# Performance work log

Hardware: AMD Instinct MI355X
Metric: run time of the kernel (lower is better)

## Reference

```python
import jax, jax.numpy as jnp
import numpy as np

TEMP = 0.07
MAX_SAMPLES = 2048
RADIUS = 10
HARD_FRAC = 0.75
FG_LABEL = 1
B, C, H, W = 8, 64, 256, 256
BLOCK = 32

MAX_FG = MAX_SAMPLES // 2                      # 1024
NEG_BUDGET = MAX_SAMPLES - MAX_FG              # 1024
HARD_BUDGET = int(round(HARD_FRAC * NEG_BUDGET))  # 768
RAND_BUDGET = NEG_BUDGET - HARD_BUDGET         # 256


def setup_inputs() -> dict:
    key = jax.random.key(0)
    feats = jax.random.normal(key, (B, C, H, W), dtype=jnp.float32)
    # 32x32-block checkerboard labels: guarantees abundant fg / ring / interior-bg pools
    ii, jj = jnp.meshgrid(jnp.arange(H), jnp.arange(W), indexing='ij')
    lbl = (((ii // BLOCK) + (jj // BLOCK)) % 2).astype(jnp.int32)
    labels = jnp.broadcast_to(lbl, (B, H, W))
    return {"feats": feats, "labels": labels}


def _forward(feats, labels):
    Bn, Cn, Hn, Wn = feats.shape
    n_pix = Hn * Wn
    f_flat = feats.reshape(Bn, Cn, n_pix).transpose(0, 2, 1)  # [B, P, C]
    l_flat = labels.reshape(Bn, n_pix)

    fg = labels == FG_LABEL                                   # [B, H, W]
    k = 2 * RADIUS + 1
    # max-pool dilation of fg mask (kernel k, stride 1, pad RADIUS == SAME)
    dil = jax.lax.reduce_window(fg.astype(jnp.float32), -jnp.inf, jax.lax.max,
                                (1, k, k), (1, 1, 1), 'SAME') > 0.0
    fg_flat = fg.reshape(Bn, n_pix)
    bg_flat = ~fg_flat                                        # all pixels valid (no ignore)
    ring_flat = dil.reshape(Bn, n_pix) & ~fg_flat & bg_flat
    bgonly_flat = bg_flat & ~ring_flat

    def per_image(f, y, fgm, ringm, bgm, key):
        k1, k2, k3 = jax.random.split(key, 3)
        def pick(mask, kk, n):
            # random subset of n true positions (== randperm[:n] in distribution)
            s = jnp.where(mask, jax.random.uniform(kk, mask.shape), -1.0)
            return jax.lax.top_k(s, n)[1]
        idx = jnp.concatenate([pick(fgm, k1, MAX_FG),
                               pick(ringm, k2, HARD_BUDGET),
                               pick(bgm, k3, RAND_BUDGET)])    # [K]
        fs = f[idx]                                            # [K, C]
        ys = y[idx]
        fs = fs / jnp.maximum(jnp.linalg.norm(fs, axis=1, keepdims=True), 1e-12)
        logits = fs @ fs.T / TEMP                              # [K, K]
        logits = logits - jax.lax.stop_gradient(logits.max(axis=1, keepdims=True))
        eye = jnp.eye(MAX_SAMPLES, dtype=bool)
        pos = (ys[:, None] == ys[None, :]) & ~eye
        exp_l = jnp.exp(logits) * (~eye)
        denom = jnp.maximum(exp_l.sum(axis=1), 1e-8)
        pos_sum = jnp.maximum(jnp.where(pos, exp_l, 0.0).sum(axis=1), 1e-8)
        valid = pos.any(axis=1) & (ys == FG_LABEL)
        loss_terms = -jnp.log(pos_sum / denom)
        n_valid = jnp.maximum(valid.sum(), 1)
        return jnp.where(valid, loss_terms, 0.0).sum() / n_valid

    keys = jax.random.split(jax.random.key(1), Bn)
    losses = jax.vmap(per_image)(f_flat, l_flat, fg_flat, ring_flat, bgonly_flat, keys)
    return losses.mean()


def reference(feats, labels):
    return _forward(feats, labels)
```

## Files before the change

### kernel.cpp

```cpp
#include <hip/hip_runtime.h>
#include <stdint.h>

#define NPIX   65536
#define NIMG   8
#define NCH    64
#define KSEL   2048
#define NFG    1024
#define NRING  768
#define NBG    256
#define INV_TEMP 14.285714285714286f

typedef __attribute__((ext_vector_type(8))) short bf16x8;
typedef __attribute__((ext_vector_type(4))) float f32x4;

__device__ __forceinline__ void tf2x32(uint32_t k0, uint32_t k1,
                                       uint32_t& x0, uint32_t& x1) {
  const uint32_t ks2 = k0 ^ k1 ^ 0x1BD11BDAu;
  x0 += k0; x1 += k1;
#define TF_RND(r) { x0 += x1; x1 = (x1 << (r)) | (x1 >> (32 - (r))); x1 ^= x0; }
  TF_RND(13) TF_RND(15) TF_RND(26) TF_RND(6)
  x0 += k1;  x1 += ks2 + 1u;
  TF_RND(17) TF_RND(29) TF_RND(16) TF_RND(24)
  x0 += ks2; x1 += k0 + 2u;
  TF_RND(13) TF_RND(15) TF_RND(26) TF_RND(6)
  x0 += k0;  x1 += k1 + 3u;
  TF_RND(17) TF_RND(29) TF_RND(16) TF_RND(24)
  x0 += k1;  x1 += ks2 + 4u;
  TF_RND(13) TF_RND(15) TF_RND(26) TF_RND(6)
  x0 += ks2; x1 += k0 + 5u;
#undef TF_RND
}

__device__ __forceinline__ ushort f2bf(float f) {
  uint32_t u = __float_as_uint(f);
  return (ushort)((u + 0x7FFFu + ((u >> 16) & 1u)) >> 16);
}

#define ZERO_F4 1552
__global__ __launch_bounds__(1024) void dilate_pack(const int* __restrict__ labels,
                                                    uint64_t* __restrict__ fgw,
                                                    uint64_t* __restrict__ dilw,
                                                    float4* __restrict__ zregion,
                                                    uint32_t* __restrict__ keys,
                                                    float* __restrict__ out) {
  __shared__ uint64_t fgs[336], hds[336];
  const int tid = threadIdx.x;
  const int img = blockIdx.x >> 2;
  const int r0 = (blockIdx.x & 3) * 64;

  if (blockIdx.x == 0) {
    for (int t = tid; t < ZERO_F4; t += 1024)
      zregion[t] = make_float4(0.f, 0.f, 0.f, 0.f);
  } else if (blockIdx.x == 1 && tid == 0) {
    out[0] = 0.0f;
    for (int b = 0; b < NIMG; ++b) {
      uint32_t kb0 = 0u, kb1 = (uint32_t)b;
      tf2x32(0u, 1u, kb0, kb1);
      for (int g = 0; g < 3; ++g) {
        uint32_t x0 = 0u, x1 = (uint32_t)g;
        tf2x32(kb0, kb1, x0, x1);
        keys[(b * 3 + g) * 2 + 0] = x0;
        keys[(b * 3 + g) * 2 + 1] = x1;
      }
    }
  }

  #pragma unroll
  for (int it = 0; it < 21; ++it) {
    int li = it * 1024 + tid;
    int hr = r0 - 10 + (li >> 8);
    int col = li & 255;
    bool bit = false;
    if (hr >= 0 && hr < 256) bit = (labels[(img << 16) + (hr << 8) + col] == 1);
    uint64_t m = __ballot(bit);
    if ((tid & 63) == 0) fgs[li >> 6] = m;
  }
  __syncthreads();

  for (int w = tid; w < 336; w += 1024) {
    int wc = w & 3;
    uint64_t x = fgs[w];
    uint64_t L = wc > 0 ? fgs[w - 1] : 0ull;
    uint64_t R = wc < 3 ? fgs[w + 1] : 0ull;
    uint64_t acc = x;
    #pragma unroll
    for (int s = 1; s <= 10; ++s) {
      acc |= (x << s) | (L >> (64 - s));
      acc |= (x >> s) | (R << (64 - s));
    }
    hds[w] = acc;
  }
  __syncthreads();

  for (int w = tid; w < 256; w += 1024) {
    int r = w >> 2, wc = w & 3;
    int gr = r0 + r;
    uint64_t acc = 0ull;
    #pragma unroll
    for (int dr = 0; dr <= 20; ++dr) acc |= hds[(r + dr) * 4 + wc];
    fgw[img * 1024 + gr * 4 + wc]  = fgs[(r + 10) * 4 + wc];
    dilw[img * 1024 + gr * 4 + wc] = acc;
  }
}

__global__ __launch_bounds__(256) void hash_hist(const uint64_t* __restrict__ fgw,
                                                 const uint64_t* __restrict__ dilw,
                                                 const uint32_t* __restrict__ keys,
                                                 uint32_t* __restrict__ mgrp,
                                                 uint32_t* __restrict__ hist) {
  __shared__ uint32_t lh[768];
  __shared__ uint64_t fgl[32], dll[32];
  const int tid = threadIdx.x;
  for (int t = tid; t < 768; t += 256) lh[t] = 0;
  const int b = blockIdx.x >> 5;
  const int base = blockIdx.x * 2048;
  const int w0 = (blockIdx.x & 31) * 32;
  if (tid < 32) fgl[tid] = fgw[b * 1024 + w0 + tid];
  else if (tid < 64) dll[tid - 32] = dilw[b * 1024 + w0 + tid - 32];
  const uint32_t K00 = keys[b * 6 + 0], K01 = keys[b * 6 + 1];
  const uint32_t K10 = keys[b * 6 + 2], K11 = keys[b * 6 + 3];
  const uint32_t K20 = keys[b * 6 + 4], K21 = keys[b * 6 + 5];
  __syncthreads();

  #pragma unroll
  for (int k = 0; k < 8; ++k) {
    int off = k * 256 + tid;
    int pix = (base + off) & 65535;
    int lw = off >> 6, bp = off & 63;
    uint32_t fgbit = (uint32_t)((fgl[lw] >> bp) & 1ull);
    uint32_t dilbit = (uint32_t)((dll[lw] >> bp) & 1ull);
    uint32_t grp = fgbit ? 0u : (dilbit ? 1u : 2u);
    uint32_t k0 = grp == 0 ? K00 : grp == 1 ? K10 : K20;
    uint32_t k1 = grp == 0 ? K01 : grp == 1 ? K11 : K21;
    uint32_t x0 = 0u, x1 = (uint32_t)pix;
    tf2x32(k0, k1, x0, x1);
    uint32_t m = (x0 ^ x1) >> 9;
    mgrp[base + off] = (m << 2) | grp;
    atomicAdd(&lh[grp * 256 + (m >> 15)], 1u);
  }
  __syncthreads();
  for (int t = tid; t < 768; t += 256)
    if (lh[t]) atomicAdd(&hist[b * 768 + t], lh[t]);
}

__global__ __launch_bounds__(256) void topk_emit(const uint32_t* __restrict__ mgrp,
                                                 const uint32_t* __restrict__ hist,
                                                 uint32_t* __restrict__ TG,
                                                 uint32_t* __restrict__ cnt,
                                                 uint32_t* __restrict__ candcnt,
                                                 unsigned long long* __restrict__ cand,
                                                 int* __restrict__ idx_out) {
  __shared__ uint32_t hh[768];
  __shared__ uint32_t sT[3], loc[3], lbd[3], basA[3], basB[3];
  const int tid = threadIdx.x;
  const int b = blockIdx.x >> 5;
  const int base = blockIdx.x * 2048;
  for (int t = tid; t < 768; t += 256) hh[t] = hist[b * 768 + t];
  if (tid < 3) { loc[tid] = 0; lbd[tid] = 0; }
  __syncthreads();

  if (tid < 3) {
    uint32_t nsel = tid == 0 ? NFG : tid == 1 ? NRING : NBG;
    const uint32_t* h = hh + tid * 256;
    uint32_t cum = 0; int T = 255;
    for (; T > 0; --T) {
      uint32_t c = h[T];
      if (cum + c >= nsel) break;
      cum += c;
    }
    sT[tid] = (uint32_t)T;
    if ((blockIdx.x & 31) == 0) {
      TG[(b * 3 + tid) * 2] = (uint32_t)T;
      TG[(b * 3 + tid) * 2 + 1] = cum;
    }
  }
  __syncthreads();
  const uint32_t T0 = sT[0], T1 = sT[1], T2 = sT[2];

  #pragma unroll
  for (int k = 0; k < 8; ++k) {
    uint32_t v = mgrp[base + k * 256 + tid];
    uint32_t g = v & 3u, bin = v >> 17;
    uint32_t T = g == 0 ? T0 : g == 1 ? T1 : T2;
    if (bin > T) atomicAdd(&loc[g], 1u);
    else if (bin == T) atomicAdd(&lbd[g], 1u);
  }
  __syncthreads();
  if (tid < 3) {
    basA[tid] = atomicAdd(&cnt[b * 3 + tid], loc[tid]);
    basB[tid] = atomicAdd(&candcnt[b * 3 + tid], lbd[tid]);
    loc[tid] = 0; lbd[tid] = 0;
  }
  __syncthreads();

  #pragma unroll
  for (int k = 0; k < 8; ++k) {
    int p = base + k * 256 + tid;
    uint32_t v = mgrp[p];
    uint32_t g = v & 3u, bin = v >> 17;
    uint32_t T = g == 0 ? T0 : g == 1 ? T1 : T2;
    int pix = p & 65535;
    if (bin > T) {
      uint32_t o = atomicAdd(&loc[g], 1u);
      int seg = g == 0 ? 0 : g == 1 ? NFG : (NFG + NRING);
      idx_out[b * KSEL + seg + (int)(basA[g] + o)] = pix;
    } else if (bin == T) {
      uint32_t o = atomicAdd(&lbd[g], 1u);
      uint32_t c = basB[g] + o;
      uint32_t m = v >> 2;
      if (c < 1024u)
        cand[(b * 3 + g) * 1024 + c] = ((unsigned long long)m << 16) | (uint32_t)pix;
    }
  }
}

#define GA 16
__global__ __launch_bounds__(256) void gather_rank_t(
    const float* __restrict__ feats, const int* __restrict__ idx,
    const uint32_t* __restrict__ TG, const uint32_t* __restrict__ candcnt,
    const unsigned long long* __restrict__ cand, ushort* __restrict__ fs) {
  __shared__ float tile[GA * 65];
  __shared__ float ssb[16 * GA];
  __shared__ float sscale[GA];
  __shared__ int lidx[GA];
  __shared__ unsigned long long cb[1024];
  const int tid = threadIdx.x;
  const int img = blockIdx.x >> 7;
  const int win = (blockIdx.x & 127) * GA;
  int seg, segoff, nsel;
  if (win < NFG)               { seg = 0; segoff = 0;            nsel = NFG; }
  else if (win < NFG + NRING)  { seg = 1; segoff = NFG;          nsel = NRING; }
  else                         { seg = 2; segoff = NFG + NRING;  nsel = NBG; }
  const int task = img * 3 + seg;
  const uint32_t G = TG[task * 2 + 1];
  const int poslo = win - segoff;

  if (tid < GA) {
    if ((uint32_t)(poslo + tid) < G)
      lidx[tid] = idx[img * KSEL + win + tid];
  }
  const bool needRank = (uint32_t)(poslo + GA) > G;
  if (needRank) {
    const int c = (int)(candcnt[task] < 1024u ? candcnt[task] : 1024u);
    const int r = nsel - (int)G;
    for (int i = tid; i < c; i += 256) cb[i] = cand[task * 1024 + i];
    __syncthreads();
    for (int i = tid; i < c; i += 256) {
      unsigned long long me = cb[i];
      uint32_t mm = (uint32_t)(me >> 16), pi = (uint32_t)(me & 0xFFFFu);
      int rank = 0;
      for (int j = 0; j < c; ++j) {
        unsigned long long o = cb[j];
        uint32_t om = (uint32_t)(o >> 16), op = (uint32_t)(o & 0xFFFFu);
        if (om > mm || (om == mm && op < pi)) ++rank;
      }
      if (rank < r) {
        int slot = (int)G + rank - poslo;
        if (slot >= 0 && slot < GA) lidx[slot] = (int)pi;
      }
    }
  }
  __syncthreads();

  const int a = tid & 15, q = tid >> 4;
  const int pix = lidx[a];
  const float* fb = feats + ((size_t)img * NCH + q * 4) * NPIX + pix;
  float ss = 0.f;
  #pragma unroll
  for (int k = 0; k < 4; ++k) {
    float v = fb[(size_t)k * NPIX];
    tile[a * 65 + q * 4 + k] = v;
    ss += v * v;
  }
  ssb[q * GA + a] = ss;
  __syncthreads();
  if (q == 0) {
    float tot = 0.f;
    #pragma unroll
    for (int q2 = 0; q2 < 16; ++q2) tot += ssb[q2 * GA + a];
    sscale[a] = 1.0f / fmaxf(sqrtf(tot), 1e-12f);
  }
  __syncthreads();

  const int row = tid >> 4, c4 = tid & 15;
  const float sc = sscale[row];
  ushort4 v4;
  v4.x = f2bf(tile[row * 65 + c4 * 4 + 0] * sc);
  v4.y = f2bf(tile[row * 65 + c4 * 4 + 1] * sc);
  v4.z = f2bf(tile[row * 65 + c4 * 4 + 2] * sc);
  v4.w = f2bf(tile[row * 65 + c4 * 4 + 3] * sc);
  ((ushort4*)(fs + ((size_t)img * KSEL + win + row) * NCH))[c4] = v4;
}

__global__ __launch_bounds__(256) void loss_mfma(const ushort* __restrict__ fs,
                                                 float* __restrict__ out) {
  const int img = blockIdx.x & 7;
  const int a0 = (blockIdx.x >> 3) * 32;
  const ushort* X = fs + (size_t)img * KSEL * NCH;
  const int tid = threadIdx.x;
  const int lane = tid & 63, wave = tid >> 6;
  const int quad = lane >> 4, col = lane & 15;
  const int rt = wave >> 1, colh = wave & 1;

  __shared__ float redD[2][2][16];
  __shared__ float redP[2][16];

  const int arow = a0 + rt * 16 + col;
  const bf16x8* Ap = (const bf16x8*)(X + (size_t)arow * NCH + quad * 8);
  const bf16x8 a_lo = Ap[0];
  const bf16x8 a_hi = Ap[4];

  float pD[4] = {0.f, 0.f, 0.f, 0.f};
  float pP[4] = {0.f, 0.f, 0.f, 0.f};
  const int ct0 = colh * 64;
  const int mbase = a0 + rt * 16 + quad * 4;

  for (int ct = ct0; ct < ct0 + 64; ++ct) {
    const int j = ct * 16 + col;
    const bf16x8* Bp = (const bf16x8*)(X + (size_t)j * NCH + quad * 8);
    bf16x8 b_lo = Bp[0];
    bf16x8 b_hi = Bp[4];
    f32x4 d = {0.f, 0.f, 0.f, 0.f};
    d = __builtin_amdgcn_mfma_f32_16x16x32_bf16(a_lo, b_lo, d, 0, 0, 0);
    d = __builtin_amdgcn_mfma_f32_16x16x32_bf16(a_hi, b_hi, d, 0, 0, 0);
    #pragma unroll
    for (int r = 0; r < 4; ++r) {
      float e = __expf(d[r] * INV_TEMP);
      if (j == mbase + r) e = 0.f;
      pD[r] += e;
      if (colh == 0) pP[r] += e;
    }
  }

  #pragma unroll
  for (int o = 1; o < 16; o <<= 1) {
    #pragma unroll
    for (int r = 0; r < 4; ++r) {
      pD[r] += __shfl_xor(pD[r], o);
      pP[r] += __shfl_xor(pP[r], o);
    }
  }
  if (col == 0) {
    #pragma unroll
    for (int r = 0; r < 4; ++r) {
      redD[rt][colh][quad * 4 + r] = pD[r];
      if (colh == 0) redP[rt][quad * 4 + r] = pP[r];
    }
  }
  __syncthreads();

  float term = 0.f;
  if (tid < 32) {
    int lrt = tid >> 4, lr = tid & 15;
    float dsum = fmaxf(redD[lrt][0][lr] + redD[lrt][1][lr], 1e-8f);
    float psum = fmaxf(redP[lrt][lr], 1e-8f);
    term = __logf(dsum) - __logf(psum);
  }
  if (tid < 64) {
    #pragma unroll
    for (int o = 32; o > 0; o >>= 1) term += __shfl_xor(term, o);
    if (tid == 0) atomicAdd(out, term * (1.0f / (NFG * NIMG)));
  }
}

extern "C" void kernel_launch(void* const* d_in, const int* in_sizes, int n_in,
                              void* d_out, int out_size, void* d_ws, size_t ws_size,
                              hipStream_t stream) {
  const float* feats = (const float*)d_in[0];
  const int* labels  = (const int*)d_in[1];
  float* out = (float*)d_out;

  char* ws = (char*)d_ws;
  uint64_t* fgw     = (uint64_t*)(ws);
  uint64_t* dilw    = (uint64_t*)(ws + 65536);
  uint32_t* keys    = (uint32_t*)(ws + 131072);
  uint32_t* TG      = (uint32_t*)(ws + 131328);
  uint32_t* hist    = (uint32_t*)(ws + 131584);
  uint32_t* cnt     = (uint32_t*)(ws + 156160);
  uint32_t* candcnt = (uint32_t*)(ws + 156288);
  unsigned long long* cand = (unsigned long long*)(ws + 156416);
  int*      idx     = (int*)(ws + 353024);
  uint32_t* mgrp    = (uint32_t*)(ws + 524288);
  ushort*   fs      = (ushort*)(ws + 2621440);

  hipLaunchKernelGGL(dilate_pack, dim3(32), dim3(1024), 0, stream,
                     labels, fgw, dilw, (float4*)hist, keys, out);
  hipLaunchKernelGGL(hash_hist, dim3(NIMG * 32), dim3(256), 0, stream,
                     fgw, dilw, keys, mgrp, hist);
  hipLaunchKernelGGL(topk_emit, dim3(NIMG * 32), dim3(256), 0, stream,
                     mgrp, hist, TG, cnt, candcnt, cand, idx);
  hipLaunchKernelGGL(gather_rank_t, dim3((NIMG * KSEL) / GA), dim3(256), 0, stream,
                     feats, idx, TG, candcnt, cand, fs);
  hipLaunchKernelGGL(loss_mfma, dim3(NIMG * (NFG / 32)), dim3(256), 0, stream,
                     fs, out);
}
```

Baseline: 243.9 us.

## Fuse dilation with hash histogram and recompute hashes in top-k emit

Merges the dilation and hash-histogram kernels into one launch that writes per-block partial histograms, and drops the global atomics on the histogram. The per-pixel mgrp buffer is removed: topk_emit recomputes the Threefry hash from the fg/dilation bitmasks instead of reading stored values. This cuts one kernel launch and the 2 MB mgrp write/read, at the cost of doing the hash twice. The fused kernel runs only 32 blocks of 1024 threads, so the hash histogram now runs on far fewer CUs than the 256 blocks used before.

```diff
diff --git a/kernel.cpp b/kernel.cpp
--- a/kernel.cpp
+++ b/kernel.cpp
@@ -31,39 +31,39 @@
 #undef TF_RND
 }
 
+__device__ __forceinline__ void img_keys(int img, uint32_t* k6) {
+  uint32_t kb0 = 0u, kb1 = (uint32_t)img;
+  tf2x32(0u, 1u, kb0, kb1);
+  #pragma unroll
+  for (int g = 0; g < 3; ++g) {
+    uint32_t x0 = 0u, x1 = (uint32_t)g;
+    tf2x32(kb0, kb1, x0, x1);
+    k6[g * 2] = x0; k6[g * 2 + 1] = x1;
+  }
+}
+
 __device__ __forceinline__ ushort f2bf(float f) {
   uint32_t u = __float_as_uint(f);
   return (ushort)((u + 0x7FFFu + ((u >> 16) & 1u)) >> 16);
 }
 
-#define ZERO_F4 1552
-__global__ __launch_bounds__(1024) void dilate_pack(const int* __restrict__ labels,
-                                                    uint64_t* __restrict__ fgw,
-                                                    uint64_t* __restrict__ dilw,
-                                                    float4* __restrict__ zregion,
-                                                    uint32_t* __restrict__ keys,
-                                                    float* __restrict__ out) {
-  __shared__ uint64_t fgs[336], hds[336];
+__global__ __launch_bounds__(1024) void dilate_hash_hist(
+    const int* __restrict__ labels, uint64_t* __restrict__ fgw,
+    uint64_t* __restrict__ dilw, uint32_t* __restrict__ histpart,
+    uint32_t* __restrict__ zsmall, float* __restrict__ out) {
+  __shared__ uint64_t fgs[336], hds[336], dls[256];
+  __shared__ uint32_t lh[768];
+  __shared__ uint32_t sk[6];
   const int tid = threadIdx.x;
   const int img = blockIdx.x >> 2;
   const int r0 = (blockIdx.x & 3) * 64;
 
   if (blockIdx.x == 0) {
-    for (int t = tid; t < ZERO_F4; t += 1024)
-      zregion[t] = make_float4(0.f, 0.f, 0.f, 0.f);
-  } else if (blockIdx.x == 1 && tid == 0) {
-    out[0] = 0.0f;
-    for (int b = 0; b < NIMG; ++b) {
-      uint32_t kb0 = 0u, kb1 = (uint32_t)b;
-      tf2x32(0u, 1u, kb0, kb1);
-      for (int g = 0; g < 3; ++g) {
-        uint32_t x0 = 0u, x1 = (uint32_t)g;
-        tf2x32(kb0, kb1, x0, x1);
-        keys[(b * 3 + g) * 2 + 0] = x0;
-        keys[(b * 3 + g) * 2 + 1] = x1;
-      }
-    }
-  }
+    if (tid < 64) zsmall[tid] = 0u;
+    if (tid == 0) out[0] = 0.0f;
+  }
+  if (tid == 0) img_keys(img, (uint32_t*)sk);
+  for (int t = tid; t < 768; t += 1024) lh[t] = 0;
 
   #pragma unroll
   for (int it = 0; it < 21; ++it) {
@@ -92,70 +92,60 @@
   }
   __syncthreads();
 
-  for (int w = tid; w < 256; w += 1024) {
-    int r = w >> 2, wc = w & 3;
-    int gr = r0 + r;
+  if (tid < 256) {
+    int r = tid >> 2, wc = tid & 3;
     uint64_t acc = 0ull;
     #pragma unroll
     for (int dr = 0; dr <= 20; ++dr) acc |= hds[(r + dr) * 4 + wc];
-    fgw[img * 1024 + gr * 4 + wc]  = fgs[(r + 10) * 4 + wc];
-    dilw[img * 1024 + gr * 4 + wc] = acc;
-  }
-}
-
-__global__ __launch_bounds__(256) void hash_hist(const uint64_t* __restrict__ fgw,
-                                                 const uint64_t* __restrict__ dilw,
-                                                 const uint32_t* __restrict__ keys,
-                                                 uint32_t* __restrict__ mgrp,
-                                                 uint32_t* __restrict__ hist) {
-  __shared__ uint32_t lh[768];
-  __shared__ uint64_t fgl[32], dll[32];
-  const int tid = threadIdx.x;
-  for (int t = tid; t < 768; t += 256) lh[t] = 0;
-  const int b = blockIdx.x >> 5;
-  const int base = blockIdx.x * 2048;
-  const int w0 = (blockIdx.x & 31) * 32;
-  if (tid < 32) fgl[tid] = fgw[b * 1024 + w0 + tid];
-  else if (tid < 64) dll[tid - 32] = dilw[b * 1024 + w0 + tid - 32];
-  const uint32_t K00 = keys[b * 6 + 0], K01 = keys[b * 6 + 1];
-  const uint32_t K10 = keys[b * 6 + 2], K11 = keys[b * 6 + 3];
-  const uint32_t K20 = keys[b * 6 + 4], K21 = keys[b * 6 + 5];
-  __syncthreads();
-
-  #pragma unroll
-  for (int k = 0; k < 8; ++k) {
-    int off = k * 256 + tid;
-    int pix = (base + off) & 65535;
-    int lw = off >> 6, bp = off & 63;
-    uint32_t fgbit = (uint32_t)((fgl[lw] >> bp) & 1ull);
-    uint32_t dilbit = (uint32_t)((dll[lw] >> bp) & 1ull);
+    dls[tid] = acc;
+    fgw[img * 1024 + (r0 + r) * 4 + wc]  = fgs[(r + 10) * 4 + wc];
+    dilw[img * 1024 + (r0 + r) * 4 + wc] = acc;
+  }
+  __syncthreads();
+
+  const uint32_t K0a = sk[0], K0b = sk[1], K1a = sk[2], K1b = sk[3],
+                 K2a = sk[4], K2b = sk[5];
+  #pragma unroll
+  for (int it = 0; it < 16; ++it) {
+    int li = it * 1024 + tid;
+    int r = li >> 8, col = li & 255;
+    int wc = col >> 6, bp = col & 63;
+    uint32_t fgbit = (uint32_t)((fgs[(r + 10) * 4 + wc] >> bp) & 1ull);
+    uint32_t dilbit = (uint32_t)((dls[r * 4 + wc] >> bp) & 1ull);
     uint32_t grp = fgbit ? 0u : (dilbit ? 1u : 2u);
-    uint32_t k0 = grp == 0 ? K00 : grp == 1 ? K10 : K20;
-    uint32_t k1 = grp == 0 ? K01 : grp == 1 ? K11 : K21;
-    uint32_t x0 = 0u, x1 = (uint32_t)pix;
+    uint32_t k0 = grp == 0 ? K0a : grp == 1 ? K1a : K2a;
+    uint32_t k1 = grp == 0 ? K0b : grp == 1 ? K1b : K2b;
+    uint32_t x0 = 0u, x1 = (uint32_t)(((r0 + r) << 8) | col);
     tf2x32(k0, k1, x0, x1);
     uint32_t m = (x0 ^ x1) >> 9;
-    mgrp[base + off] = (m << 2) | grp;
     atomicAdd(&lh[grp * 256 + (m >> 15)], 1u);
   }
   __syncthreads();
-  for (int t = tid; t < 768; t += 256)
-    if (lh[t]) atomicAdd(&hist[b * 768 + t], lh[t]);
-}
-
-__global__ __launch_bounds__(256) void topk_emit(const uint32_t* __restrict__ mgrp,
-                                                 const uint32_t* __restrict__ hist,
-                                                 uint32_t* __restrict__ TG,
-                                                 uint32_t* __restrict__ cnt,
-                                                 uint32_t* __restrict__ candcnt,
-                                                 unsigned long long* __restrict__ cand,
-                                                 int* __restrict__ idx_out) {
+  for (int t = tid; t < 768; t += 1024)
+    histpart[blockIdx.x * 768 + t] = lh[t];
+}
+
+__global__ __launch_bounds__(256) void topk_emit(
+    const uint64_t* __restrict__ fgw, const uint64_t* __restrict__ dilw,
+    const uint32_t* __restrict__ histpart, uint32_t* __restrict__ TG,
+    uint32_t* __restrict__ cnt, uint32_t* __restrict__ candcnt,
+    unsigned long long* __restrict__ cand, int* __restrict__ idx_out) {
   __shared__ uint32_t hh[768];
+  __shared__ uint64_t fgl[32], dll[32];
+  __shared__ uint32_t sk[6];
   __shared__ uint32_t sT[3], loc[3], lbd[3], basA[3], basB[3];
   const int tid = threadIdx.x;
   const int b = blockIdx.x >> 5;
   const int base = blockIdx.x * 2048;
-  for (int t = tid; t < 768; t += 256) hh[t] = hist[b * 768 + t];
+  const int w0 = (blockIdx.x & 31) * 32;
+
+  for (int t = tid; t < 768; t += 256) {
+    const uint32_t* hp = histpart + (b * 4) * 768 + t;
+    hh[t] = hp[0] + hp[768] + hp[1536] + hp[2304];
+  }
+  if (tid == 0) img_keys(b, (uint32_t*)sk);
+  if (tid < 32) fgl[tid] = fgw[b * 1024 + w0 + tid];
+  else if (tid < 64) dll[tid - 32] = dilw[b * 1024 + w0 + tid - 32];
   if (tid < 3) { loc[tid] = 0; lbd[tid] = 0; }
   __syncthreads();
 
@@ -175,15 +165,26 @@
     }
   }
   __syncthreads();
-  const uint32_t T0 = sT[0], T1 = sT[1], T2 = sT[2];
-
+
+  uint32_t mv[8]; uint32_t gv[8];
+  const uint32_t K0a = sk[0], K0b = sk[1], K1a = sk[2], K1b = sk[3],
+                 K2a = sk[4], K2b = sk[5];
   #pragma unroll
   for (int k = 0; k < 8; ++k) {
-    uint32_t v = mgrp[base + k * 256 + tid];
-    uint32_t g = v & 3u, bin = v >> 17;
-    uint32_t T = g == 0 ? T0 : g == 1 ? T1 : T2;
-    if (bin > T) atomicAdd(&loc[g], 1u);
-    else if (bin == T) atomicAdd(&lbd[g], 1u);
+    int off = k * 256 + tid;
+    int lw = off >> 6, bp = off & 63;
+    uint32_t fgbit = (uint32_t)((fgl[lw] >> bp) & 1ull);
+    uint32_t dilbit = (uint32_t)((dll[lw] >> bp) & 1ull);
+    uint32_t grp = fgbit ? 0u : (dilbit ? 1u : 2u);
+    uint32_t k0 = grp == 0 ? K0a : grp == 1 ? K1a : K2a;
+    uint32_t k1 = grp == 0 ? K0b : grp == 1 ? K1b : K2b;
+    uint32_t x0 = 0u, x1 = (uint32_t)((base + off) & 65535);
+    tf2x32(k0, k1, x0, x1);
+    uint32_t m = (x0 ^ x1) >> 9;
+    mv[k] = m; gv[k] = grp;
+    uint32_t T = sT[grp], bin = m >> 15;
+    if (bin > T) atomicAdd(&loc[grp], 1u);
+    else if (bin == T) atomicAdd(&lbd[grp], 1u);
   }
   __syncthreads();
   if (tid < 3) {
@@ -195,11 +196,9 @@
 
   #pragma unroll
   for (int k = 0; k < 8; ++k) {
-    int p = base + k * 256 + tid;
-    uint32_t v = mgrp[p];
-    uint32_t g = v & 3u, bin = v >> 17;
-    uint32_t T = g == 0 ? T0 : g == 1 ? T1 : T2;
-    int pix = p & 65535;
+    uint32_t m = mv[k], g = gv[k];
+    uint32_t T = sT[g], bin = m >> 15;
+    int pix = (base + k * 256 + tid) & 65535;
     if (bin > T) {
       uint32_t o = atomicAdd(&loc[g], 1u);
       int seg = g == 0 ? 0 : g == 1 ? NFG : (NFG + NRING);
@@ -207,7 +206,6 @@
     } else if (bin == T) {
       uint32_t o = atomicAdd(&lbd[g], 1u);
       uint32_t c = basB[g] + o;
-      uint32_t m = v >> 2;
       if (c < 1024u)
         cand[(b * 3 + g) * 1024 + c] = ((unsigned long long)m << 16) | (uint32_t)pix;
     }
@@ -371,24 +369,20 @@
   float* out = (float*)d_out;
 
   char* ws = (char*)d_ws;
-  uint64_t* fgw     = (uint64_t*)(ws);
-  uint64_t* dilw    = (uint64_t*)(ws + 65536);
-  uint32_t* keys    = (uint32_t*)(ws + 131072);
-  uint32_t* TG      = (uint32_t*)(ws + 131328);
-  uint32_t* hist    = (uint32_t*)(ws + 131584);
-  uint32_t* cnt     = (uint32_t*)(ws + 156160);
-  uint32_t* candcnt = (uint32_t*)(ws + 156288);
-  unsigned long long* cand = (unsigned long long*)(ws + 156416);
-  int*      idx     = (int*)(ws + 353024);
-  uint32_t* mgrp    = (uint32_t*)(ws + 524288);
-  ushort*   fs      = (ushort*)(ws + 2621440);
-
-  hipLaunchKernelGGL(dilate_pack, dim3(32), dim3(1024), 0, stream,
-                     labels, fgw, dilw, (float4*)hist, keys, out);
-  hipLaunchKernelGGL(hash_hist, dim3(NIMG * 32), dim3(256), 0, stream,
-                     fgw, dilw, keys, mgrp, hist);
+  uint64_t* fgw      = (uint64_t*)(ws);
+  uint64_t* dilw     = (uint64_t*)(ws + 65536);
+  uint32_t* histpart = (uint32_t*)(ws + 131072);
+  uint32_t* TG       = (uint32_t*)(ws + 229376);
+  uint32_t* cnt      = (uint32_t*)(ws + 229632);
+  uint32_t* candcnt  = (uint32_t*)(ws + 229760);
+  unsigned long long* cand = (unsigned long long*)(ws + 229888);
+  int*      idx      = (int*)(ws + 426496);
+  ushort*   fs       = (ushort*)(ws + 524288);
+
+  hipLaunchKernelGGL(dilate_hash_hist, dim3(32), dim3(1024), 0, stream,
+                     labels, fgw, dilw, histpart, cnt, out);
   hipLaunchKernelGGL(topk_emit, dim3(NIMG * 32), dim3(256), 0, stream,
-                     mgrp, hist, TG, cnt, candcnt, cand, idx);
+                     fgw, dilw, histpart, TG, cnt, candcnt, cand, idx);
   hipLaunchKernelGGL(gather_rank_t, dim3((NIMG * KSEL) / GA), dim3(256), 0, stream,
                      feats, idx, TG, candcnt, cand, fs);
   hipLaunchKernelGGL(loss_mfma, dim3(NIMG * (NFG / 32)), dim3(256), 0, stream,
```

Result: no change. 244.9 us (+0.4%).
